# Kernel tuning notes

Measured on AMD Instinct MI355X. Metric: run time of the kernel, lower is better.

The kernel has to match this reference:

```python
import jax, jax.numpy as jnp
import numpy as np

# Problem dims (see shape_source)
T, H, FFN, K, E = 2048, 1024, 2048, 4, 32
LOCAL_EXPERT_IDS = (0, 8, 16, 24)  # round_robin plan: E=32, ep_size=8, ep_rank=0
N_LOCAL = len(LOCAL_EXPERT_IDS)
W_INIT = 0.02


def setup_inputs() -> dict:
    key = jax.random.key(0)
    k1, k2, k3, k4, k5 = jax.random.split(key, 5)
    hidden_2d = jax.random.normal(k1, (T, H), jnp.float32)
    selected_experts = jax.random.randint(k2, (T, K), 0, E)          # int routing ids
    routing_weights = jax.random.uniform(k3, (T, K), jnp.float32)    # nonneg gate probs
    gate_up_stack = jax.random.normal(k4, (N_LOCAL, 2 * FFN, H), jnp.float32) * W_INIT
    down_stack = jax.random.normal(k5, (N_LOCAL, H, FFN), jnp.float32) * W_INIT
    return {
        "hidden_2d": hidden_2d,
        "selected_experts": selected_experts,
        "routing_weights": routing_weights,
        "gate_up_stack": gate_up_stack,
        "down_stack": down_stack,
    }


def reference(hidden_2d, selected_experts, routing_weights, gate_up_stack, down_stack):
    """JAX port of ShardedExperts.forward_local.

    Same math as the torch sort/gather grouped-GEMM path: for every
    (token, k) assignment whose expert id is local, compute
    down(silu(gate) * up) and scatter-add routing_weight * out into the
    token row. Expressed densely per local expert (fixed small loop),
    which is the jit-friendly equivalent: the per-token expert weight
    w_e[t] = sum_k routing_weights[t,k] * [selected[t,k] == e] collapses
    duplicate assignments exactly like index_add_ does.
    """
    partial = jnp.zeros_like(hidden_2d)
    for i, eid in enumerate(LOCAL_EXPERT_IDS):
        # [T] combined routing weight for this expert (0 for unrouted tokens)
        w_e = jnp.sum(routing_weights * (selected_experts == eid), axis=-1)
        gu = hidden_2d @ gate_up_stack[i].T          # [T, 2*FFN]
        gate, up = jnp.split(gu, 2, axis=-1)         # gu.chunk(2, dim=-1)
        h = jax.nn.silu(gate) * up                   # act_fn(gate) * up
        out = h @ down_stack[i].T                    # [T, H]
        partial = partial + out * w_e[:, None]
    return partial
```

## Files before the change

### kernel.cpp

```cpp
#include <hip/hip_runtime.h>
#include <cstdint>
#include <cstddef>

#define TT  2048
#define HH  1024
#define FFN 2048
#define NL  4
#define BK  64
#define BM  256

typedef __attribute__((ext_vector_type(8))) short bf16x8;
typedef __attribute__((ext_vector_type(4))) float f32x4;
typedef __attribute__((ext_vector_type(2))) float f32x2;

__device__ __forceinline__ unsigned short f2bf(float f) {
  unsigned u = __builtin_bit_cast(unsigned, f);
  u += 0x7FFFu + ((u >> 16) & 1u);
  return (unsigned short)(u >> 16);
}

__device__ __forceinline__ bf16x8 pack8(f32x4 f0, f32x4 f1) {
  bf16x8 v;
  v[0] = (short)f2bf(f0[0]); v[1] = (short)f2bf(f0[1]);
  v[2] = (short)f2bf(f0[2]); v[3] = (short)f2bf(f0[3]);
  v[4] = (short)f2bf(f1[0]); v[5] = (short)f2bf(f1[1]);
  v[6] = (short)f2bf(f1[2]); v[7] = (short)f2bf(f1[3]);
  return v;
}

__device__ __forceinline__ unsigned pack2(f32x2 f) {
  return (unsigned)f2bf(f[0]) | ((unsigned)f2bf(f[1]) << 16);
}

__device__ __forceinline__ void async16(void* lds, const void* g) {
  __builtin_amdgcn_global_load_lds(
      (const __attribute__((address_space(1))) unsigned int*)g,
      (__attribute__((address_space(3))) unsigned int*)lds, 16, 0, 0);
}

__device__ __forceinline__ int swz(int b) { return b ^ (((b >> 7) & 7) << 4); }

__device__ __forceinline__ void lds_barrier() {
  asm volatile("s_waitcnt lgkmcnt(0)" ::: "memory");
  __builtin_amdgcn_s_barrier();
}

__global__ void k_zero(float* __restrict__ out, int* __restrict__ cnt) {
  int i = blockIdx.x * 256 + threadIdx.x;
  f32x4 z = {0.f, 0.f, 0.f, 0.f};
  reinterpret_cast<f32x4*>(out)[i] = z;
  if (i < NL) cnt[i] = 0;
}

__global__ void k_build(const int* __restrict__ sel, const float* __restrict__ rw,
                        int* __restrict__ cnt, int* __restrict__ tok,
                        float* __restrict__ wgt) {
  int t = blockIdx.x * 256 + threadIdx.x;
  if (t >= TT) return;
  int   s0 = sel[t*4+0], s1 = sel[t*4+1], s2 = sel[t*4+2], s3 = sel[t*4+3];
  float r0 = rw[t*4+0],  r1 = rw[t*4+1],  r2 = rw[t*4+2],  r3 = rw[t*4+3];
#pragma unroll
  for (int i = 0; i < NL; ++i) {
    int eid = i * 8;
    float w = 0.f; bool m = false;
    if (s0 == eid) { w += r0; m = true; }
    if (s1 == eid) { w += r1; m = true; }
    if (s2 == eid) { w += r2; m = true; }
    if (s3 == eid) { w += r3; m = true; }
    if (m) {
      int p = atomicAdd(&cnt[i], 1);
      tok[i*TT + p] = t;
      wgt[i*TT + p] = w;
    }
  }
}

__global__ void k_gather(const float* __restrict__ hidden, const int* __restrict__ cnt,
                         const int* __restrict__ tok, unsigned short* __restrict__ X) {
  int p = blockIdx.x, e = blockIdx.y;
  if (p >= cnt[e]) return;
  int t = tok[e*TT + p];
  const f32x4* src = reinterpret_cast<const f32x4*>(hidden + (size_t)t * HH);
  f32x4 a = src[threadIdx.x*2], b = src[threadIdx.x*2 + 1];
  reinterpret_cast<bf16x8*>(X + ((size_t)e*TT + p) * HH)[threadIdx.x] = pack8(a, b);
}

__global__ __launch_bounds__(512) void k_gemm1(
    const unsigned short* __restrict__ X, const float* __restrict__ gup,
    const int* __restrict__ cnt, unsigned short* __restrict__ Hb) {
  int bid = blockIdx.x;
  int xcd = bid & 7;
  int e   = xcd >> 1;
  int idx = (bid >> 3) * 2 + (xcd & 1);
  int n0  = idx * 32;
  int c   = cnt[e];

  __shared__ alignas(16) unsigned short As[4][BM*BK];
  __shared__ alignas(16) unsigned short Bs[2][64*BK];

  int tid  = threadIdx.x;
  int lane = tid & 63, wv = tid >> 6;
  int lr = lane & 15,  lk = lane >> 4;
  int wm = wv >> 1,    wn = wv & 1;

  const unsigned short* Ab = X   + (size_t)e * TT * HH;
  const float*          Gb = gup + (size_t)e * 2 * FFN * HH;

  int arow[4], acol[4], dstA[4];
#pragma unroll
  for (int cc = 0; cc < 4; ++cc) {
    int chunk = wv * 4 + cc;
    int P = chunk * 1024 + lane * 16;
    arow[cc] = P >> 7;
    acol[cc] = (P & 127) ^ ((arow[cc] & 7) << 4);
    dstA[cc] = P;
  }

  int rb  = tid >> 3;
  int cbf = (tid & 7) * 8;
  int grow = (rb < 32) ? (n0 + rb) : (FFN + n0 + rb - 32);
  const float* gB = Gb + (size_t)grow * HH + cbf;
  int wb = swz(rb * 128 + cbf * 2);

  int aoff[4][2], bgo[2], buo[2];
#pragma unroll
  for (int mi = 0; mi < 4; ++mi)
#pragma unroll
    for (int kk = 0; kk < 2; ++kk)
      aoff[mi][kk] = swz((wm*64 + mi*16 + lr) * 128 + kk*64 + lk*16);
#pragma unroll
  for (int kk = 0; kk < 2; ++kk) {
    bgo[kk] = swz((wn*16 + lr) * 128 + kk*64 + lk*16);
    buo[kk] = swz((32 + wn*16 + lr) * 128 + kk*64 + lk*16);
  }

  const int NT = HH / BK;

  for (int m0 = 0; m0 < c; m0 += BM) {
    __syncthreads();

    const char* srcA[4];
#pragma unroll
    for (int cc = 0; cc < 4; ++cc)
      srcA[cc] = (const char*)(Ab + (size_t)(m0 + arow[cc]) * HH) + acol[cc];

    f32x4 accg[4], accu[4];
    f32x4 z = {0.f, 0.f, 0.f, 0.f};
#pragma unroll
    for (int a = 0; a < 4; ++a) { accg[a] = z; accu[a] = z; }

    f32x4 br[3][2];

    br[0][0] = *(const f32x4*)(gB);
    br[0][1] = *(const f32x4*)(gB + 4);
#pragma unroll
    for (int cc = 0; cc < 4; ++cc) async16((char*)As[0] + dstA[cc], srcA[cc]);
#pragma unroll
    for (int cc = 0; cc < 4; ++cc) async16((char*)As[1] + dstA[cc], srcA[cc] + BK*2);
#pragma unroll
    for (int cc = 0; cc < 4; ++cc) async16((char*)As[2] + dstA[cc], srcA[cc] + 2*BK*2);
    br[1][0] = *(const f32x4*)(gB + BK);
    br[1][1] = *(const f32x4*)(gB + BK + 4);
    br[2][0] = *(const f32x4*)(gB + 2*BK);
    br[2][1] = *(const f32x4*)(gB + 2*BK + 4);
    *(bf16x8*)((char*)Bs[0] + wb) = pack8(br[0][0], br[0][1]);
    asm volatile("s_waitcnt vmcnt(12)" ::: "memory");
    lds_barrier();

#pragma unroll
    for (int t = 0; t < NT; ++t) {
      if (t + 3 < NT) {
        int k3 = (t + 3) * BK;
#pragma unroll
        for (int cc = 0; cc < 4; ++cc)
          async16((char*)As[(t+3) & 3] + dstA[cc], srcA[cc] + k3*2);
        br[(t+3) % 3][0] = *(const f32x4*)(gB + k3);
        br[(t+3) % 3][1] = *(const f32x4*)(gB + k3 + 4);
      }
      __builtin_amdgcn_sched_barrier(0);
      {
        const char* Asc = (const char*)As[t & 3];
        const char* Bsc = (const char*)Bs[t & 1];
#pragma unroll
        for (int kk = 0; kk < 2; ++kk) {
          bf16x8 bg = *(const bf16x8*)(Bsc + bgo[kk]);
          bf16x8 bu = *(const bf16x8*)(Bsc + buo[kk]);
#pragma unroll
          for (int mi = 0; mi < 4; ++mi) {
            bf16x8 a = *(const bf16x8*)(Asc + aoff[mi][kk]);
            accg[mi] = __builtin_amdgcn_mfma_f32_16x16x32_bf16(a, bg, accg[mi], 0, 0, 0);
            accu[mi] = __builtin_amdgcn_mfma_f32_16x16x32_bf16(a, bu, accu[mi], 0, 0, 0);
          }
        }
      }
      if (t + 1 < NT) {
        *(bf16x8*)((char*)Bs[(t+1) & 1] + wb) =
            pack8(br[(t+1) % 3][0], br[(t+1) % 3][1]);
        lds_barrier();
      }
    }

#pragma unroll
    for (int mi = 0; mi < 4; ++mi)
#pragma unroll
      for (int j = 0; j < 4; ++j) {
        int p = m0 + wm*64 + mi*16 + lk*4 + j;
        if (p < c) {
          float gv = accg[mi][j];
          float hv = (gv / (1.f + __expf(-gv))) * accu[mi][j];
          Hb[((size_t)e * TT + p) * FFN + (n0 + wn*16 + lr)] = f2bf(hv);
        }
      }
  }
}

__global__ __launch_bounds__(512) void k_gemm2(
    const unsigned short* __restrict__ Hb, const float* __restrict__ down,
    const int* __restrict__ cnt, const int* __restrict__ tok,
    const float* __restrict__ wgt, float* __restrict__ out) {
  int bid = blockIdx.x;
  int xcd = bid & 7;
  int e   = xcd >> 1;
  int idx = (bid >> 3) * 2 + (xcd & 1);
  int n0  = idx * 16;
  int c   = cnt[e];

  __shared__ alignas(16) unsigned short As[4][BM*BK];
  __shared__ alignas(16) unsigned short Bs[2][16*BK];

  int tid  = threadIdx.x;
  int lane = tid & 63, wv = tid >> 6;
  int lr = lane & 15,  lk = lane >> 4;

  const unsigned short* Ab = Hb   + (size_t)e * TT * FFN;
  const float*          Db = down + (size_t)e * HH * FFN;

  int arow[4], acol[4], dstA[4];
#pragma unroll
  for (int cc = 0; cc < 4; ++cc) {
    int chunk = wv * 4 + cc;
    int P = chunk * 1024 + lane * 16;
    arow[cc] = P >> 7;
    acol[cc] = (P & 127) ^ ((arow[cc] & 7) << 4);
    dstA[cc] = P;
  }

  int rb = tid >> 5;
  int cw = tid & 31;
  const float* gB = Db + (size_t)(n0 + rb) * FFN + cw*2;
  int wb = swz(rb * 128 + cw * 4);

  int aoff[2][2], boff[2];
#pragma unroll
  for (int mi = 0; mi < 2; ++mi)
#pragma unroll
    for (int kk = 0; kk < 2; ++kk)
      aoff[mi][kk] = swz((wv*32 + mi*16 + lr) * 128 + kk*64 + lk*16);
#pragma unroll
  for (int kk = 0; kk < 2; ++kk)
    boff[kk] = swz((lr) * 128 + kk*64 + lk*16);

  const int NT = FFN / BK;

  for (int m0 = 0; m0 < c; m0 += BM) {
    __syncthreads();

    const char* srcA[4];
#pragma unroll
    for (int cc = 0; cc < 4; ++cc)
      srcA[cc] = (const char*)(Ab + (size_t)(m0 + arow[cc]) * FFN) + acol[cc];

    f32x4 acc[2];
    f32x4 z = {0.f, 0.f, 0.f, 0.f};
    acc[0] = z; acc[1] = z;

    f32x2 br[3];

    br[0] = *(const f32x2*)(gB);
#pragma unroll
    for (int cc = 0; cc < 4; ++cc) async16((char*)As[0] + dstA[cc], srcA[cc]);
#pragma unroll
    for (int cc = 0; cc < 4; ++cc) async16((char*)As[1] + dstA[cc], srcA[cc] + BK*2);
#pragma unroll
    for (int cc = 0; cc < 4; ++cc) async16((char*)As[2] + dstA[cc], srcA[cc] + 2*BK*2);
    br[1] = *(const f32x2*)(gB + BK);
    br[2] = *(const f32x2*)(gB + 2*BK);
    *(unsigned*)((char*)Bs[0] + wb) = pack2(br[0]);
    asm volatile("s_waitcnt vmcnt(10)" ::: "memory");
    lds_barrier();

#pragma unroll
    for (int t = 0; t < NT; ++t) {
      if (t + 3 < NT) {
        int k3 = (t + 3) * BK;
#pragma unroll
        for (int cc = 0; cc < 4; ++cc)
          async16((char*)As[(t+3) & 3] + dstA[cc], srcA[cc] + k3*2);
        br[(t+3) % 3] = *(const f32x2*)(gB + k3);
      }
      __builtin_amdgcn_sched_barrier(0);
      {
        const char* Asc = (const char*)As[t & 3];
        const char* Bsc = (const char*)Bs[t & 1];
#pragma unroll
        for (int kk = 0; kk < 2; ++kk) {
          bf16x8 bf_ = *(const bf16x8*)(Bsc + boff[kk]);
#pragma unroll
          for (int mi = 0; mi < 2; ++mi) {
            bf16x8 a = *(const bf16x8*)(Asc + aoff[mi][kk]);
            acc[mi] = __builtin_amdgcn_mfma_f32_16x16x32_bf16(a, bf_, acc[mi], 0, 0, 0);
          }
        }
      }
      if (t + 1 < NT) {
        *(unsigned*)((char*)Bs[(t+1) & 1] + wb) = pack2(br[(t+1) % 3]);
        lds_barrier();
      }
    }

#pragma unroll
    for (int mi = 0; mi < 2; ++mi)
#pragma unroll
      for (int j = 0; j < 4; ++j) {
        int p = m0 + wv*32 + mi*16 + lk*4 + j;
        if (p < c) {
          int   t = tok[e*TT + p];
          float w = wgt[e*TT + p];
          atomicAdd(&out[(size_t)t * HH + (n0 + lr)], w * acc[mi][j]);
        }
      }
  }
}

extern "C" void kernel_launch(void* const* d_in, const int* in_sizes, int n_in,
                              void* d_out, int out_size, void* d_ws, size_t ws_size,
                              hipStream_t stream) {
  const float* hidden = (const float*)d_in[0];
  const int*   sel    = (const int*)d_in[1];
  const float* rw     = (const float*)d_in[2];
  const float* gup    = (const float*)d_in[3];
  const float* dwn    = (const float*)d_in[4];
  float* out = (float*)d_out;

  char* ws = (char*)d_ws;
  int*            cnt  = (int*)ws;
  int*            tok  = (int*)(ws + 1024);
  float*          wgt  = (float*)(ws + 33792);
  unsigned short* X    = (unsigned short*)(ws + 66560);
  unsigned short* Hb   = (unsigned short*)(ws + 16843776);

  k_zero  <<<2048, 256, 0, stream>>>(out, cnt);
  k_build <<<8,    256, 0, stream>>>(sel, rw, cnt, tok, wgt);
  k_gather<<<dim3(TT, NL), 128, 0, stream>>>(hidden, cnt, tok, X);
  k_gemm1 <<<256, 512, 0, stream>>>(X, gup, cnt, Hb);
  k_gemm2 <<<256, 512, 0, stream>>>(Hb, dwn, cnt, tok, wgt, out);
}
```

Before: 58.20 us.

## Split-K gemm2 across two blocks and load A directly into registers

The down-projection kernel now splits the FFN reduction in half, doubling the grid to 512 blocks, and relies on the existing atomicAdd output to combine the partial sums. The A tile is no longer staged through shared memory with async copies. Each lane reads its MFMA fragments straight from global memory into double-buffered registers, which removes the large As LDS buffer and should raise occupancy. The trade-off is twice the atomic traffic, uncoalesced per-lane A loads, and a loss of the XCD-aware block mapping.

```diff
diff --git a/kernel.cpp b/kernel.cpp
--- a/kernel.cpp
+++ b/kernel.cpp
@@ -8,6 +8,7 @@
 #define NL  4
 #define BK  64
 #define BM  256
+#define SK2 2
 
 typedef __attribute__((ext_vector_type(8))) short bf16x8;
 typedef __attribute__((ext_vector_type(4))) float f32x4;
@@ -219,101 +220,88 @@
     const int* __restrict__ cnt, const int* __restrict__ tok,
     const float* __restrict__ wgt, float* __restrict__ out) {
   int bid = blockIdx.x;
-  int xcd = bid & 7;
-  int e   = xcd >> 1;
-  int idx = (bid >> 3) * 2 + (xcd & 1);
-  int n0  = idx * 16;
+  int e   = bid & 3;
+  int sk  = (bid >> 2) & 1;
+  int n0  = (bid >> 3) * 16;
   int c   = cnt[e];
-
-  __shared__ alignas(16) unsigned short As[4][BM*BK];
+  int kbase = sk * (FFN / SK2);
+
   __shared__ alignas(16) unsigned short Bs[2][16*BK];
 
   int tid  = threadIdx.x;
   int lane = tid & 63, wv = tid >> 6;
   int lr = lane & 15,  lk = lane >> 4;
 
-  const unsigned short* Ab = Hb   + (size_t)e * TT * FFN;
+  const unsigned short* Ab = Hb   + (size_t)e * TT * FFN + kbase;
   const float*          Db = down + (size_t)e * HH * FFN;
-
-  int arow[4], acol[4], dstA[4];
-#pragma unroll
-  for (int cc = 0; cc < 4; ++cc) {
-    int chunk = wv * 4 + cc;
-    int P = chunk * 1024 + lane * 16;
-    arow[cc] = P >> 7;
-    acol[cc] = (P & 127) ^ ((arow[cc] & 7) << 4);
-    dstA[cc] = P;
-  }
 
   int rb = tid >> 5;
   int cw = tid & 31;
-  const float* gB = Db + (size_t)(n0 + rb) * FFN + cw*2;
+  const float* gB = Db + (size_t)(n0 + rb) * FFN + kbase + cw*2;
   int wb = swz(rb * 128 + cw * 4);
 
-  int aoff[2][2], boff[2];
-#pragma unroll
-  for (int mi = 0; mi < 2; ++mi)
-#pragma unroll
-    for (int kk = 0; kk < 2; ++kk)
-      aoff[mi][kk] = swz((wv*32 + mi*16 + lr) * 128 + kk*64 + lk*16);
+  int boff[2];
 #pragma unroll
   for (int kk = 0; kk < 2; ++kk)
     boff[kk] = swz((lr) * 128 + kk*64 + lk*16);
 
-  const int NT = FFN / BK;
+  const int NT = (FFN / SK2) / BK;
 
   for (int m0 = 0; m0 < c; m0 += BM) {
     __syncthreads();
 
-    const char* srcA[4];
-#pragma unroll
-    for (int cc = 0; cc < 4; ++cc)
-      srcA[cc] = (const char*)(Ab + (size_t)(m0 + arow[cc]) * FFN) + acol[cc];
+    const unsigned short* Arow[2];
+#pragma unroll
+    for (int mi = 0; mi < 2; ++mi)
+      Arow[mi] = Ab + (size_t)(m0 + wv*32 + mi*16 + lr) * FFN + lk*8;
 
     f32x4 acc[2];
     f32x4 z = {0.f, 0.f, 0.f, 0.f};
     acc[0] = z; acc[1] = z;
 
-    f32x2 br[3];
-
-    br[0] = *(const f32x2*)(gB);
-#pragma unroll
-    for (int cc = 0; cc < 4; ++cc) async16((char*)As[0] + dstA[cc], srcA[cc]);
-#pragma unroll
-    for (int cc = 0; cc < 4; ++cc) async16((char*)As[1] + dstA[cc], srcA[cc] + BK*2);
-#pragma unroll
-    for (int cc = 0; cc < 4; ++cc) async16((char*)As[2] + dstA[cc], srcA[cc] + 2*BK*2);
-    br[1] = *(const f32x2*)(gB + BK);
-    br[2] = *(const f32x2*)(gB + 2*BK);
-    *(unsigned*)((char*)Bs[0] + wb) = pack2(br[0]);
-    asm volatile("s_waitcnt vmcnt(10)" ::: "memory");
-    lds_barrier();
+    bf16x8 aS[2][4];
+    f32x2  br[2];
+
+    {
+      f32x2 b0 = *(const f32x2*)(gB);
+      *(unsigned*)((char*)Bs[0] + wb) = pack2(b0);
+#pragma unroll
+      for (int mi = 0; mi < 2; ++mi)
+#pragma unroll
+        for (int kk = 0; kk < 2; ++kk) {
+          aS[0][mi*2+kk] = *(const bf16x8*)(Arow[mi] + kk*32);
+          aS[1][mi*2+kk] = *(const bf16x8*)(Arow[mi] + BK + kk*32);
+        }
+      br[1] = *(const f32x2*)(gB + BK);
+      lds_barrier();
+    }
 
 #pragma unroll
     for (int t = 0; t < NT; ++t) {
-      if (t + 3 < NT) {
-        int k3 = (t + 3) * BK;
-#pragma unroll
-        for (int cc = 0; cc < 4; ++cc)
-          async16((char*)As[(t+3) & 3] + dstA[cc], srcA[cc] + k3*2);
-        br[(t+3) % 3] = *(const f32x2*)(gB + k3);
-      }
+      if (t + 2 < NT)
+        br[t & 1] = *(const f32x2*)(gB + (t + 2) * BK);
       __builtin_amdgcn_sched_barrier(0);
       {
-        const char* Asc = (const char*)As[t & 3];
         const char* Bsc = (const char*)Bs[t & 1];
 #pragma unroll
         for (int kk = 0; kk < 2; ++kk) {
           bf16x8 bf_ = *(const bf16x8*)(Bsc + boff[kk]);
 #pragma unroll
-          for (int mi = 0; mi < 2; ++mi) {
-            bf16x8 a = *(const bf16x8*)(Asc + aoff[mi][kk]);
-            acc[mi] = __builtin_amdgcn_mfma_f32_16x16x32_bf16(a, bf_, acc[mi], 0, 0, 0);
-          }
-        }
+          for (int mi = 0; mi < 2; ++mi)
+            acc[mi] = __builtin_amdgcn_mfma_f32_16x16x32_bf16(
+                aS[t & 1][mi*2+kk], bf_, acc[mi], 0, 0, 0);
+        }
+      }
+      if (t + 2 < NT) {
+        int k2 = (t + 2) * BK;
+#pragma unroll
+        for (int mi = 0; mi < 2; ++mi)
+#pragma unroll
+          for (int kk = 0; kk < 2; ++kk)
+            aS[t & 1][mi*2+kk] = *(const bf16x8*)(Arow[mi] + k2 + kk*32);
       }
       if (t + 1 < NT) {
-        *(unsigned*)((char*)Bs[(t+1) & 1] + wb) = pack2(br[(t+1) % 3]);
+        *(unsigned*)((char*)Bs[(t+1) & 1] + wb) = pack2(br[(t+1) & 1]);
         lds_barrier();
       }
     }
@@ -353,5 +341,5 @@
   k_build <<<8,    256, 0, stream>>>(sel, rw, cnt, tok, wgt);
   k_gather<<<dim3(TT, NL), 128, 0, stream>>>(hidden, cnt, tok, X);
   k_gemm1 <<<256, 512, 0, stream>>>(X, gup, cnt, Hb);
-  k_gemm2 <<<256, 512, 0, stream>>>(Hb, dwn, cnt, tok, wgt, out);
-}
+  k_gemm2 <<<512, 512, 0, stream>>>(Hb, dwn, cnt, tok, wgt, out);
+}
```

Result: slower. 71.61 us (+23.0%).

## Widen gemm2 N tile to 32 and split K in two across blocks

Applied to the files above, without the earlier changes.

The down-projection kernel now computes a 32-column output tile per block, with waves arranged 4x2 over M and N so each wave does 4 MFMAs per B fragment. The FFN reduction is split into two halves handled by separate blocks, which combine through the existing atomicAdd output path. Each A tile loaded into LDS now feeds twice as many output columns, and the B fp32 loads become 16-byte vectors. The trade-off is twice as many atomic adds to the output, and grid size must match the new block-index decoding.

```diff
diff --git a/kernel.cpp b/kernel.cpp
--- a/kernel.cpp
+++ b/kernel.cpp
@@ -8,10 +8,11 @@
 #define NL  4
 #define BK  64
 #define BM  256
+#define SK2 2
 
 typedef __attribute__((ext_vector_type(8))) short bf16x8;
+typedef __attribute__((ext_vector_type(4))) unsigned short u16x4;
 typedef __attribute__((ext_vector_type(4))) float f32x4;
-typedef __attribute__((ext_vector_type(2))) float f32x2;
 
 __device__ __forceinline__ unsigned short f2bf(float f) {
   unsigned u = __builtin_bit_cast(unsigned, f);
@@ -28,8 +29,10 @@
   return v;
 }
 
-__device__ __forceinline__ unsigned pack2(f32x2 f) {
-  return (unsigned)f2bf(f[0]) | ((unsigned)f2bf(f[1]) << 16);
+__device__ __forceinline__ u16x4 pack4(f32x4 f) {
+  u16x4 v;
+  v[0] = f2bf(f[0]); v[1] = f2bf(f[1]); v[2] = f2bf(f[2]); v[3] = f2bf(f[3]);
+  return v;
 }
 
 __device__ __forceinline__ void async16(void* lds, const void* g) {
@@ -222,17 +225,20 @@
   int xcd = bid & 7;
   int e   = xcd >> 1;
   int idx = (bid >> 3) * 2 + (xcd & 1);
-  int n0  = idx * 16;
+  int sk  = idx >> 5;
+  int n0  = (idx & 31) * 32;
   int c   = cnt[e];
+  int kbase = sk * (FFN / SK2);
 
   __shared__ alignas(16) unsigned short As[4][BM*BK];
-  __shared__ alignas(16) unsigned short Bs[2][16*BK];
+  __shared__ alignas(16) unsigned short Bs[2][32*BK];
 
   int tid  = threadIdx.x;
   int lane = tid & 63, wv = tid >> 6;
   int lr = lane & 15,  lk = lane >> 4;
-
-  const unsigned short* Ab = Hb   + (size_t)e * TT * FFN;
+  int wm = wv >> 1,    wn = wv & 1;
+
+  const unsigned short* Ab = Hb   + (size_t)e * TT * FFN + kbase;
   const float*          Db = down + (size_t)e * HH * FFN;
 
   int arow[4], acol[4], dstA[4];
@@ -245,22 +251,22 @@
     dstA[cc] = P;
   }
 
-  int rb = tid >> 5;
-  int cw = tid & 31;
-  const float* gB = Db + (size_t)(n0 + rb) * FFN + cw*2;
-  int wb = swz(rb * 128 + cw * 4);
-
-  int aoff[2][2], boff[2];
-#pragma unroll
-  for (int mi = 0; mi < 2; ++mi)
+  int rb  = tid >> 4;
+  int cbf = (tid & 15) * 4;
+  const float* gB = Db + (size_t)(n0 + rb) * FFN + kbase + cbf;
+  int wb = swz(rb * 128 + cbf * 2);
+
+  int aoff[4][2], boff[2];
+#pragma unroll
+  for (int mi = 0; mi < 4; ++mi)
 #pragma unroll
     for (int kk = 0; kk < 2; ++kk)
-      aoff[mi][kk] = swz((wv*32 + mi*16 + lr) * 128 + kk*64 + lk*16);
+      aoff[mi][kk] = swz((wm*64 + mi*16 + lr) * 128 + kk*64 + lk*16);
 #pragma unroll
   for (int kk = 0; kk < 2; ++kk)
-    boff[kk] = swz((lr) * 128 + kk*64 + lk*16);
-
-  const int NT = FFN / BK;
+    boff[kk] = swz((wn*16 + lr) * 128 + kk*64 + lk*16);
+
+  const int NT = (FFN / SK2) / BK;
 
   for (int m0 = 0; m0 < c; m0 += BM) {
     __syncthreads();
@@ -270,22 +276,23 @@
     for (int cc = 0; cc < 4; ++cc)
       srcA[cc] = (const char*)(Ab + (size_t)(m0 + arow[cc]) * FFN) + acol[cc];
 
-    f32x4 acc[2];
+    f32x4 acc[4];
     f32x4 z = {0.f, 0.f, 0.f, 0.f};
-    acc[0] = z; acc[1] = z;
-
-    f32x2 br[3];
-
-    br[0] = *(const f32x2*)(gB);
+#pragma unroll
+    for (int a = 0; a < 4; ++a) acc[a] = z;
+
+    f32x4 br[3];
+
+    br[0] = *(const f32x4*)(gB);
 #pragma unroll
     for (int cc = 0; cc < 4; ++cc) async16((char*)As[0] + dstA[cc], srcA[cc]);
 #pragma unroll
     for (int cc = 0; cc < 4; ++cc) async16((char*)As[1] + dstA[cc], srcA[cc] + BK*2);
 #pragma unroll
     for (int cc = 0; cc < 4; ++cc) async16((char*)As[2] + dstA[cc], srcA[cc] + 2*BK*2);
-    br[1] = *(const f32x2*)(gB + BK);
-    br[2] = *(const f32x2*)(gB + 2*BK);
-    *(unsigned*)((char*)Bs[0] + wb) = pack2(br[0]);
+    br[1] = *(const f32x4*)(gB + BK);
+    br[2] = *(const f32x4*)(gB + 2*BK);
+    *(u16x4*)((char*)Bs[0] + wb) = pack4(br[0]);
     asm volatile("s_waitcnt vmcnt(10)" ::: "memory");
     lds_barrier();
 
@@ -296,7 +303,7 @@
 #pragma unroll
         for (int cc = 0; cc < 4; ++cc)
           async16((char*)As[(t+3) & 3] + dstA[cc], srcA[cc] + k3*2);
-        br[(t+3) % 3] = *(const f32x2*)(gB + k3);
+        br[(t+3) % 3] = *(const f32x4*)(gB + k3);
       }
       __builtin_amdgcn_sched_barrier(0);
       {
@@ -306,27 +313,27 @@
         for (int kk = 0; kk < 2; ++kk) {
           bf16x8 bf_ = *(const bf16x8*)(Bsc + boff[kk]);
 #pragma unroll
-          for (int mi = 0; mi < 2; ++mi) {
+          for (int mi = 0; mi < 4; ++mi) {
             bf16x8 a = *(const bf16x8*)(Asc + aoff[mi][kk]);
             acc[mi] = __builtin_amdgcn_mfma_f32_16x16x32_bf16(a, bf_, acc[mi], 0, 0, 0);
           }
         }
       }
       if (t + 1 < NT) {
-        *(unsigned*)((char*)Bs[(t+1) & 1] + wb) = pack2(br[(t+1) % 3]);
+        *(u16x4*)((char*)Bs[(t+1) & 1] + wb) = pack4(br[(t+1) % 3]);
         lds_barrier();
       }
     }
 
 #pragma unroll
-    for (int mi = 0; mi < 2; ++mi)
+    for (int mi = 0; mi < 4; ++mi)
 #pragma unroll
       for (int j = 0; j < 4; ++j) {
-        int p = m0 + wv*32 + mi*16 + lk*4 + j;
+        int p = m0 + wm*64 + mi*16 + lk*4 + j;
         if (p < c) {
           int   t = tok[e*TT + p];
           float w = wgt[e*TT + p];
-          atomicAdd(&out[(size_t)t * HH + (n0 + lr)], w * acc[mi][j]);
+          atomicAdd(&out[(size_t)t * HH + (n0 + wn*16 + lr)], w * acc[mi][j]);
         }
       }
   }
```

Measured after the change: 56.01 us. -3.7%, faster.
